# Kernel tuning notes

Hardware: AMD Instinct MI355X
Metric: run time of the kernel (lower is better)

The kernel has to match this reference:

```python
import jax, jax.numpy as jnp
import numpy as np

N_NODES = 50000
N_EDGES = 800000
BATCH = 4
D = 64


def setup_inputs() -> dict:
    key = jax.random.key(0)
    ks = jax.random.split(key, 8)
    state = jax.random.normal(ks[0], (BATCH, N_NODES, D), dtype=jnp.float32)
    edge_row = jax.random.randint(ks[1], (N_EDGES,), 0, N_NODES, dtype=jnp.int32)
    edge_col = jax.random.randint(ks[2], (N_EDGES,), 0, N_NODES, dtype=jnp.int32)
    edge_weight = jax.random.uniform(ks[3], (N_EDGES,), dtype=jnp.float32)
    stdv = 1.0 / np.sqrt(D)
    W1 = jax.random.uniform(ks[4], (D, D), minval=-stdv, maxval=stdv, dtype=jnp.float32)
    b1 = jnp.zeros((D,), dtype=jnp.float32)
    W2 = jax.random.uniform(ks[5], (D, D), minval=-stdv, maxval=stdv, dtype=jnp.float32)
    b2 = jnp.zeros((D,), dtype=jnp.float32)
    w_out = jax.random.normal(ks[6], (D,), dtype=jnp.float32) * stdv
    return {"state": state, "edge_row": edge_row, "edge_col": edge_col,
            "edge_weight": edge_weight, "W1": W1, "b1": b1, "W2": W2,
            "b2": b2, "w_out": w_out}


def _gcn_layer(x, W, bias, edge_row, edge_col, edge_weight, n, b):
    # x: [n, b, d_in] -> support [n, b, d_out]
    support = jnp.einsum('nbk,kp->nbp', x, W) + bias
    flat = support.reshape(n, -1)  # [n, b*d_out]
    # sparse spmm: out[i] = sum_{e: row_e=i} w_e * flat[col_e]
    msgs = edge_weight[:, None] * flat[edge_col]  # [E, b*d_out]
    out = jax.ops.segment_sum(msgs, edge_row, num_segments=n)
    return jax.nn.relu(out.reshape(n, b, -1))


def reference(state, edge_row, edge_col, edge_weight, W1, b1, W2, b2, w_out):
    b, n, _ = state.shape
    x = jnp.transpose(state, (1, 0, 2))  # [n, b, d]
    for W, bias in ((W1, b1), (W2, b2)):
        x = _gcn_layer(x, W, bias, edge_row, edge_col, edge_weight, n, b)
    # actor head: Linear(d,1,bias=False), squeeze, transpose -> [b, n]
    logits = jnp.einsum('nbd,d->nb', x, w_out)
    return logits.T
```

## Files before the change

kernel.cpp:

```cpp
#include <hip/hip_runtime.h>


typedef _Float16 fp16_t;
typedef _Float16 h4 __attribute__((ext_vector_type(4)));
typedef _Float16 h8 __attribute__((ext_vector_type(8)));
typedef float    f4 __attribute__((ext_vector_type(4)));
typedef unsigned long long ull;

#define CAP   64
#define RPB   256
#define BCAP  4608
#define CHK   3200
#define LROW  264
#define S1Q   (127.f / 4.f)
#define S1D   (4.f / 127.f)

__global__ __launch_bounds__(64) void prepW_k(const float* __restrict__ W,
                                              const float* __restrict__ bias,
                                              fp16_t* __restrict__ wf,
                                              float* __restrict__ bf,
                                              int* __restrict__ gcnt, int NB) {
    int lane = threadIdx.x;
    for (int i = lane; i < NB; i += 64) gcnt[i] = 0;
    int r16 = lane & 15, half = lane >> 4;
#pragma unroll
    for (int kk = 0; kk < 2; ++kk)
#pragma unroll
        for (int j = 0; j < 4; ++j) {
            h8 v;
#pragma unroll
            for (int t = 0; t < 8; ++t)
                v[t] = (_Float16)W[(32 * kk + 8 * half + t) * 64 + 16 * j + r16];
            *(h8*)&wf[((kk * 4 + j) * 64 + lane) * 8] = v;
        }
#pragma unroll
    for (int j = 0; j < 4; ++j) bf[j * 64 + lane] = bias[16 * j + r16];
}

__global__ __launch_bounds__(256) void bg_k(const int* __restrict__ erow,
                                            const int* __restrict__ ecol,
                                            const float* __restrict__ ew,
                                            int* __restrict__ gcnt,
                                            ull* __restrict__ bed,
                                            int E, int NB, int NB1,
                                            const float* __restrict__ xf,
                                            const float* __restrict__ W,
                                            const float* __restrict__ bias,
                                            unsigned char* __restrict__ flat1,
                                            int N) {
    if ((int)blockIdx.x < NB1) {
        __shared__ int hist[256], offs[256], cur[256], gbase[256];
        __shared__ ull stage[CHK];
        __shared__ unsigned short sbkt[CHK];
        int tid = threadIdx.x;
        int e0 = blockIdx.x * CHK;
        int e1 = e0 + CHK < E ? e0 + CHK : E;

        hist[tid] = 0;
        cur[tid] = 0;
        __syncthreads();
        for (int e = e0 + tid; e < e1; e += 256)
            atomicAdd(&hist[erow[e] >> 8], 1);
        __syncthreads();
        int v = hist[tid];
        offs[tid] = v;
        __syncthreads();
        for (int off = 1; off < 256; off <<= 1) {
            int t = (tid >= off) ? offs[tid - off] : 0;
            __syncthreads();
            offs[tid] += t;
            __syncthreads();
        }
        offs[tid] -= v;
        if (tid < NB && v > 0) gbase[tid] = atomicAdd(&gcnt[tid], v);
        __syncthreads();
        for (int e = e0 + tid; e < e1; e += 256) {
            int r = erow[e];
            int bk = r >> 8;
            unsigned q = (unsigned)(ew[e] * 32767.f + 0.5f);
            ull pv = ((ull)(r & 255) << 32) | (q << 17) | (unsigned)ecol[e];
            int idx = offs[bk] + atomicAdd(&cur[bk], 1);
            stage[idx] = pv;
            sbkt[idx] = (unsigned short)bk;
        }
        __syncthreads();
        int total = e1 - e0;
        for (int i = tid; i < total; i += 256) {
            int bk = sbkt[i];
            int sl = gbase[bk] + (i - offs[bk]);
            if (sl < BCAP) bed[(size_t)bk * BCAP + sl] = stage[i];
        }
    } else {
        int wave = threadIdx.x >> 6;
        int lane = threadIdx.x & 63;
        int r16 = lane & 15, half = lane >> 4;

        h8 Bf[2][4];
#pragma unroll
        for (int kk = 0; kk < 2; ++kk)
#pragma unroll
            for (int j = 0; j < 4; ++j) {
                h8 v;
#pragma unroll
                for (int t = 0; t < 8; ++t)
                    v[t] = (_Float16)W[(32 * kk + 8 * half + t) * 64 + 16 * j + r16];
                Bf[kk][j] = v;
            }
        float bj[4];
#pragma unroll
        for (int j = 0; j < 4; ++j) bj[j] = bias[16 * j + r16];

        int ntile = N >> 4;
        int gstride = gridDim.x - NB1;
        for (int tile = blockIdx.x - NB1; tile < ntile; tile += gstride) {
            int row = tile * 16 + r16;
            const float* p = xf + ((size_t)wave * N + row) * 64 + 8 * half;
            f4 u0 = *(const f4*)p;
            f4 u1 = *(const f4*)(p + 4);
            f4 u2 = *(const f4*)(p + 32);
            f4 u3 = *(const f4*)(p + 36);
            h8 A0, A1;
#pragma unroll
            for (int t = 0; t < 4; ++t) {
                A0[t] = (_Float16)u0[t]; A0[t + 4] = (_Float16)u1[t];
                A1[t] = (_Float16)u2[t]; A1[t + 4] = (_Float16)u3[t];
            }
#pragma unroll
            for (int j = 0; j < 4; ++j) {
                f4 c = {0.f, 0.f, 0.f, 0.f};
                c = __builtin_amdgcn_mfma_f32_16x16x32_f16(A0, Bf[0][j], c, 0, 0, 0);
                c = __builtin_amdgcn_mfma_f32_16x16x32_f16(A1, Bf[1][j], c, 0, 0, 0);
#pragma unroll
                for (int r = 0; r < 4; ++r) {
                    int orow = tile * 16 + 4 * half + r;
                    float fu = fmaf(c[r] + bj[j], S1Q, 128.f);
                    fu = fminf(fmaxf(fu, 0.f), 255.f);
                    flat1[(size_t)orow * 256 + wave * 64 + 16 * j + r16] =
                        (unsigned char)(fu + 0.5f);
                }
            }
        }
    }
}

__global__ __launch_bounds__(1024) void build2_k(const ull* __restrict__ bed,
                                                 const int* __restrict__ gcnt,
                                                 unsigned* __restrict__ ed,
                                                 int* __restrict__ cnt, int N) {
    __shared__ unsigned sbuf[RPB * CAP];
    __shared__ int scnt[RPB];
    int b = blockIdx.x, tid = threadIdx.x;
    for (int i = tid; i < RPB * CAP; i += 1024) sbuf[i] = 0;
    if (tid < RPB) scnt[tid] = 0;
    __syncthreads();
    int n = gcnt[b];
    n = n < BCAP ? n : BCAP;
    const ull* p = bed + (size_t)b * BCAP;
    for (int i = tid; i < n; i += 1024) {
        ull v = p[i];
        int rl = (int)(v >> 32);
        int pos = atomicAdd(&scnt[rl], 1);
        if (pos < CAP) sbuf[(rl << 6) + pos] = (unsigned)v;
    }
    __syncthreads();
    size_t base = (size_t)b * (RPB * CAP);
    for (int i = tid; i < RPB * CAP; i += 1024)
        ed[base + i] = sbuf[i];
    int r = b * RPB + tid;
    if (tid < RPB && r < N) cnt[r] = scnt[tid] < CAP ? scnt[tid] : CAP;
}

#define EDGE4I(pk, A0, A1, A2, A3, WS)                                         \
    {                                                                          \
        unsigned _p = (pk);                                                    \
        float _w = (float)(_p >> 17) * (1.f / 32767.f);                        \
        unsigned _v = *(const unsigned*)(fb + ((size_t)(_p & 0x1FFFFu) << 8)   \
                                         + lane4);                             \
        A0 += _w * (float)(_v & 0xffu);                                        \
        A1 += _w * (float)((_v >> 8) & 0xffu);                                 \
        A2 += _w * (float)((_v >> 16) & 0xffu);                                \
        A3 += _w * (float)(_v >> 24);                                          \
        WS += _w;                                                              \
    }

__global__ __launch_bounds__(256) void spmmG_k(const unsigned char* __restrict__ flat,
                                               const int* __restrict__ cnt,
                                               const unsigned* __restrict__ ed,
                                               const fp16_t* __restrict__ wf,
                                               const float* __restrict__ bf,
                                               unsigned char* __restrict__ flat2i,
                                               float* __restrict__ s2, int N) {
    __shared__ fp16_t sagg[16 * LROW];
    __shared__ h8     swf[8 * 64];
    __shared__ float  sbf[4 * 64];
    int tid  = threadIdx.x;
    int wave = tid >> 6;
    int lane = tid & 63;
    int lane4 = lane * 4;
    int r16 = lane & 15, half = lane >> 4;

    ((f4*)swf)[tid] = ((const f4*)wf)[tid];
    ((f4*)swf)[tid + 256] = ((const f4*)wf)[tid + 256];
    sbf[tid] = bf[tid];

    int blk0 = blockIdx.x * 16;
    const char* fb = (const char*)flat;
    int r0 = blk0 + wave * 4;

    int mm0 = __builtin_amdgcn_readfirstlane(cnt[r0]);
    int mm1 = __builtin_amdgcn_readfirstlane(cnt[r0 + 1]);
    int mm2 = __builtin_amdgcn_readfirstlane(cnt[r0 + 2]);
    int mm3 = __builtin_amdgcn_readfirstlane(cnt[r0 + 3]);
#define C4(a, b) ((((a) > (b) ? (a) : (b)) + 3) & ~3)
    int cA = C4(mm0, mm1) + C4(mm2, mm3);
    int cB = C4(mm0, mm2) + C4(mm1, mm3);
    int cC = C4(mm0, mm3) + C4(mm1, mm2);
    int i1, i2, i3, mI1, mI2, mI3;
    if (cA <= cB && cA <= cC) { i1 = 1; i2 = 2; i3 = 3; mI1 = mm1; mI2 = mm2; mI3 = mm3; }
    else if (cB <= cC)        { i1 = 2; i2 = 1; i3 = 3; mI1 = mm2; mI2 = mm1; mI3 = mm3; }
    else                      { i1 = 3; i2 = 1; i3 = 2; mI1 = mm3; mI2 = mm1; mI3 = mm2; }

    int pa[2] = {0, i2}, pb[2] = {i1, i3};
    int pma[2] = {mm0, mI2}, pmb[2] = {mI1, mI3};
#pragma unroll
    for (int pr = 0; pr < 2; ++pr) {
        int la = pa[pr], lb = pb[pr];
        int mr = C4(pma[pr], pmb[pr]);
        const unsigned* e0 = ed + (size_t)(r0 + la) * CAP;
        const unsigned* e1 = ed + (size_t)(r0 + lb) * CAP;
        float a0 = 0.f, a1 = 0.f, a2 = 0.f, a3 = 0.f, wsA = 0.f;
        float c0 = 0.f, c1 = 0.f, c2 = 0.f, c3 = 0.f, wsC = 0.f;
        for (int j = 0; j < mr; j += 4) {
            uint4 pA = *(const uint4*)(e0 + j);
            uint4 pB = *(const uint4*)(e1 + j);
            EDGE4I(pA.x, a0, a1, a2, a3, wsA) EDGE4I(pB.x, c0, c1, c2, c3, wsC)
            EDGE4I(pA.y, a0, a1, a2, a3, wsA) EDGE4I(pB.y, c0, c1, c2, c3, wsC)
            EDGE4I(pA.z, a0, a1, a2, a3, wsA) EDGE4I(pB.z, c0, c1, c2, c3, wsC)
            EDGE4I(pA.w, a0, a1, a2, a3, wsA) EDGE4I(pB.w, c0, c1, c2, c3, wsC)
        }
        float bA = 128.f * wsA, bC = 128.f * wsC;
        h4 s0, s1;
        s0.x = (fp16_t)fmaxf(S1D * (a0 - bA), 0.f);
        s0.y = (fp16_t)fmaxf(S1D * (a1 - bA), 0.f);
        s0.z = (fp16_t)fmaxf(S1D * (a2 - bA), 0.f);
        s0.w = (fp16_t)fmaxf(S1D * (a3 - bA), 0.f);
        s1.x = (fp16_t)fmaxf(S1D * (c0 - bC), 0.f);
        s1.y = (fp16_t)fmaxf(S1D * (c1 - bC), 0.f);
        s1.z = (fp16_t)fmaxf(S1D * (c2 - bC), 0.f);
        s1.w = (fp16_t)fmaxf(S1D * (c3 - bC), 0.f);
        *(h4*)&sagg[(wave * 4 + la) * LROW + lane4] = s0;
        *(h4*)&sagg[(wave * 4 + lb) * LROW + lane4] = s1;
    }
#undef C4
    __syncthreads();

    h8 A0 = *(const h8*)&sagg[r16 * LROW + wave * 64 + 8 * half];
    h8 A1 = *(const h8*)&sagg[r16 * LROW + wave * 64 + 32 + 8 * half];
    f4 cc[4];
#pragma unroll
    for (int j = 0; j < 4; ++j) {
        f4 c = {0.f, 0.f, 0.f, 0.f};
        c = __builtin_amdgcn_mfma_f32_16x16x32_f16(A0, swf[j * 64 + lane], c, 0, 0, 0);
        c = __builtin_amdgcn_mfma_f32_16x16x32_f16(A1, swf[(4 + j) * 64 + lane], c, 0, 0, 0);
        float bjv = sbf[j * 64 + lane];
        c.x += bjv; c.y += bjv; c.z += bjv; c.w += bjv;
        cc[j] = c;
    }
#pragma unroll
    for (int r = 0; r < 4; ++r) {
        float m = fmaxf(fmaxf(fabsf(cc[0][r]), fabsf(cc[1][r])),
                        fmaxf(fabsf(cc[2][r]), fabsf(cc[3][r])));
        m = fmaxf(m, __shfl_xor(m, 1));
        m = fmaxf(m, __shfl_xor(m, 2));
        m = fmaxf(m, __shfl_xor(m, 4));
        m = fmaxf(m, __shfl_xor(m, 8));
        int orow = blk0 + 4 * half + r;
        float inv = (m > 0.f) ? (127.f / m) : 0.f;
        if (r16 == 0) s2[(orow << 2) | wave] = m * (1.f / 127.f);
#pragma unroll
        for (int j = 0; j < 4; ++j) {
            float q = fmaf(cc[j][r], inv, 128.f);
            flat2i[(size_t)orow * 256 + wave * 64 + 16 * j + r16] =
                (unsigned char)(q + 0.5f);
        }
    }
}

#define EDGE4Q(pk, A0, A1, A2, A3, WS)                                         \
    {                                                                          \
        unsigned _p = (pk);                                                    \
        unsigned _c = _p & 0x1FFFFu;                                           \
        float _w = (float)(_p >> 17) * (1.f / 32767.f) * s2[(_c << 2) | bsel]; \
        unsigned _v = *(const unsigned*)(fb + ((size_t)_c << 8) + lane4);      \
        A0 += _w * (float)(_v & 0xffu);                                        \
        A1 += _w * (float)((_v >> 8) & 0xffu);                                 \
        A2 += _w * (float)((_v >> 16) & 0xffu);                                \
        A3 += _w * (float)(_v >> 24);                                          \
        WS += _w;                                                              \
    }

__global__ __launch_bounds__(256) void spmm2h_k(const unsigned char* __restrict__ flat,
                                                const int* __restrict__ cnt,
                                                const unsigned* __restrict__ ed,
                                                const float* __restrict__ s2,
                                                const float* __restrict__ wout,
                                                float* __restrict__ out, int N) {
    int rowi = blockIdx.x * 4 + (int)(threadIdx.x >> 6);
    int lane = threadIdx.x & 63;
    int lane4 = lane * 4;
    int bsel = lane >> 4;
    const char* fb = (const char*)flat;
    int m = __builtin_amdgcn_readfirstlane(cnt[rowi]);
    int mr = (m + 7) & ~7;
    const unsigned* ep = ed + (size_t)rowi * CAP;
    float a0 = 0.f, a1 = 0.f, a2 = 0.f, a3 = 0.f, ws = 0.f;
    for (int j = 0; j < mr; j += 8) {
        uint4 pA = *(const uint4*)(ep + j);
        uint4 pB = *(const uint4*)(ep + j + 4);
        EDGE4Q(pA.x, a0, a1, a2, a3, ws) EDGE4Q(pA.y, a0, a1, a2, a3, ws)
        EDGE4Q(pA.z, a0, a1, a2, a3, ws) EDGE4Q(pA.w, a0, a1, a2, a3, ws)
        EDGE4Q(pB.x, a0, a1, a2, a3, ws) EDGE4Q(pB.y, a0, a1, a2, a3, ws)
        EDGE4Q(pB.z, a0, a1, a2, a3, ws) EDGE4Q(pB.w, a0, a1, a2, a3, ws)
    }
    float bs = 128.f * ws;
    int t = lane & 15;
    float4 wo = ((const float4*)wout)[t];
    float p = fmaxf(a0 - bs, 0.f) * wo.x + fmaxf(a1 - bs, 0.f) * wo.y +
              fmaxf(a2 - bs, 0.f) * wo.z + fmaxf(a3 - bs, 0.f) * wo.w;
    p += __shfl_xor(p, 1); p += __shfl_xor(p, 2);
    p += __shfl_xor(p, 4); p += __shfl_xor(p, 8);
    if (t == 0) out[(size_t)bsel * N + rowi] = p;
}

extern "C" void kernel_launch(void* const* d_in, const int* in_sizes, int n_in,
                              void* d_out, int out_size, void* d_ws, size_t ws_size,
                              hipStream_t stream) {
    const float* state = (const float*)d_in[0];
    const int*   erow  = (const int*)d_in[1];
    const int*   ecol  = (const int*)d_in[2];
    const float* ew    = (const float*)d_in[3];
    const float* W1    = (const float*)d_in[4];
    const float* b1    = (const float*)d_in[5];
    const float* W2    = (const float*)d_in[6];
    const float* b2    = (const float*)d_in[7];
    const float* wout  = (const float*)d_in[8];
    float* out = (float*)d_out;

    int N = in_sizes[0] / (4 * 64);
    int E = in_sizes[1];
    int NB = (N + RPB - 1) / RPB;

    char* ws = (char*)d_ws;
    size_t off = 0;
    auto alloc = [&](size_t bytes) -> char* {
        char* p = ws + off;
        off += (bytes + 255) & ~(size_t)255;
        return p;
    };
    unsigned char* flat1  = (unsigned char*)alloc((size_t)N * 256);
    unsigned char* flat2i = (unsigned char*)alloc((size_t)N * 256);
    float*    s2    = (float*)alloc((size_t)N * 4 * 4);
    int*      cnt   = (int*)alloc((size_t)NB * RPB * 4);
    unsigned* ed    = (unsigned*)alloc((size_t)NB * RPB * CAP * 4);
    int*      gcnt  = (int*)alloc((size_t)NB * 4);
    ull*      bed   = (ull*)alloc((size_t)NB * BCAP * 8);
    fp16_t*   wf    = (fp16_t*)alloc(8 * 64 * 8 * 2);
    float*    bfr   = (float*)alloc(4 * 64 * 4);
    if (off > ws_size) return;

    prepW_k<<<1, 64, 0, stream>>>(W2, b2, wf, bfr, gcnt, NB);
    int nblk1 = (E + CHK - 1) / CHK;
    bg_k<<<nblk1 + 1024, 256, 0, stream>>>(erow, ecol, ew, gcnt, bed, E, NB,
                                           nblk1, state, W1, b1, flat1, N);
    build2_k<<<NB, 1024, 0, stream>>>(bed, gcnt, ed, cnt, N);
    spmmG_k<<<N / 16, 256, 0, stream>>>(flat1, cnt, ed, wf, bfr, flat2i, s2, N);
    spmm2h_k<<<(N + 3) / 4, 256, 0, stream>>>(flat2i, cnt, ed, s2, wout, out, N);
}
```

Baseline: 106.2 us.

## Fold W2 prep into bg_k, precompute per-row weight sums, drop per-edge scale multiplies

The separate prepW_k launch is removed. The W2/bias fp16 repacking now runs in an extra block of bg_k, and gcnt is zeroed with hipMemsetAsync. build2_k now accumulates each row's quantized edge-weight sum into a new sumq buffer, so spmmG_k no longer keeps a per-edge weight-sum accumulator. The 1/32767 dequant factor is folded into the final scale constants and into s2, which removes a multiply per edge in both SpMM kernels. The cost is an extra LDS atomic per edge in build2_k and a memset launch in place of the kernel launch. The weight sum now also includes edges beyond CAP, which the kept edge list drops.

```diff
diff --git a/kernel.cpp b/kernel.cpp
--- a/kernel.cpp
+++ b/kernel.cpp
@@ -14,28 +14,7 @@
 #define LROW  264
 #define S1Q   (127.f / 4.f)
 #define S1D   (4.f / 127.f)
-
-__global__ __launch_bounds__(64) void prepW_k(const float* __restrict__ W,
-                                              const float* __restrict__ bias,
-                                              fp16_t* __restrict__ wf,
-                                              float* __restrict__ bf,
-                                              int* __restrict__ gcnt, int NB) {
-    int lane = threadIdx.x;
-    for (int i = lane; i < NB; i += 64) gcnt[i] = 0;
-    int r16 = lane & 15, half = lane >> 4;
-#pragma unroll
-    for (int kk = 0; kk < 2; ++kk)
-#pragma unroll
-        for (int j = 0; j < 4; ++j) {
-            h8 v;
-#pragma unroll
-            for (int t = 0; t < 8; ++t)
-                v[t] = (_Float16)W[(32 * kk + 8 * half + t) * 64 + 16 * j + r16];
-            *(h8*)&wf[((kk * 4 + j) * 64 + lane) * 8] = v;
-        }
-#pragma unroll
-    for (int j = 0; j < 4; ++j) bf[j * 64 + lane] = bias[16 * j + r16];
-}
+#define SC1   (4.f / (127.f * 32767.f))
 
 __global__ __launch_bounds__(256) void bg_k(const int* __restrict__ erow,
                                             const int* __restrict__ ecol,
@@ -44,10 +23,33 @@
                                             ull* __restrict__ bed,
                                             int E, int NB, int NB1,
                                             const float* __restrict__ xf,
-                                            const float* __restrict__ W,
-                                            const float* __restrict__ bias,
+                                            const float* __restrict__ W1,
+                                            const float* __restrict__ b1,
                                             unsigned char* __restrict__ flat1,
+                                            const float* __restrict__ W2,
+                                            const float* __restrict__ b2,
+                                            fp16_t* __restrict__ wf,
+                                            float* __restrict__ bf,
                                             int N) {
+    if ((int)blockIdx.x == NB1) {
+        int lane = threadIdx.x;
+        if (lane < 64) {
+            int r16 = lane & 15, half = lane >> 4;
+#pragma unroll
+            for (int kk = 0; kk < 2; ++kk)
+#pragma unroll
+                for (int j = 0; j < 4; ++j) {
+                    h8 v;
+#pragma unroll
+                    for (int t = 0; t < 8; ++t)
+                        v[t] = (_Float16)W2[(32 * kk + 8 * half + t) * 64 + 16 * j + r16];
+                    *(h8*)&wf[((kk * 4 + j) * 64 + lane) * 8] = v;
+                }
+#pragma unroll
+            for (int j = 0; j < 4; ++j) bf[j * 64 + lane] = b2[16 * j + r16];
+        }
+        return;
+    }
     if ((int)blockIdx.x < NB1) {
         __shared__ int hist[256], offs[256], cur[256], gbase[256];
         __shared__ ull stage[CHK];
@@ -103,16 +105,16 @@
                 h8 v;
 #pragma unroll
                 for (int t = 0; t < 8; ++t)
-                    v[t] = (_Float16)W[(32 * kk + 8 * half + t) * 64 + 16 * j + r16];
+                    v[t] = (_Float16)W1[(32 * kk + 8 * half + t) * 64 + 16 * j + r16];
                 Bf[kk][j] = v;
             }
         float bj[4];
 #pragma unroll
-        for (int j = 0; j < 4; ++j) bj[j] = bias[16 * j + r16];
+        for (int j = 0; j < 4; ++j) bj[j] = b1[16 * j + r16];
 
         int ntile = N >> 4;
-        int gstride = gridDim.x - NB1;
-        for (int tile = blockIdx.x - NB1; tile < ntile; tile += gstride) {
+        int gstride = gridDim.x - NB1 - 1;
+        for (int tile = blockIdx.x - NB1 - 1; tile < ntile; tile += gstride) {
             int row = tile * 16 + r16;
             const float* p = xf + ((size_t)wave * N + row) * 64 + 8 * half;
             f4 u0 = *(const f4*)p;
@@ -146,12 +148,14 @@
 __global__ __launch_bounds__(1024) void build2_k(const ull* __restrict__ bed,
                                                  const int* __restrict__ gcnt,
                                                  unsigned* __restrict__ ed,
-                                                 int* __restrict__ cnt, int N) {
+                                                 int* __restrict__ cnt,
+                                                 int* __restrict__ sumq, int N) {
     __shared__ unsigned sbuf[RPB * CAP];
     __shared__ int scnt[RPB];
+    __shared__ int ssum[RPB];
     int b = blockIdx.x, tid = threadIdx.x;
     for (int i = tid; i < RPB * CAP; i += 1024) sbuf[i] = 0;
-    if (tid < RPB) scnt[tid] = 0;
+    if (tid < RPB) { scnt[tid] = 0; ssum[tid] = 0; }
     __syncthreads();
     int n = gcnt[b];
     n = n < BCAP ? n : BCAP;
@@ -159,32 +163,37 @@
     for (int i = tid; i < n; i += 1024) {
         ull v = p[i];
         int rl = (int)(v >> 32);
+        unsigned pk = (unsigned)v;
         int pos = atomicAdd(&scnt[rl], 1);
-        if (pos < CAP) sbuf[(rl << 6) + pos] = (unsigned)v;
+        if (pos < CAP) sbuf[(rl << 6) + pos] = pk;
+        atomicAdd(&ssum[rl], (int)(pk >> 17));
     }
     __syncthreads();
     size_t base = (size_t)b * (RPB * CAP);
     for (int i = tid; i < RPB * CAP; i += 1024)
         ed[base + i] = sbuf[i];
     int r = b * RPB + tid;
-    if (tid < RPB && r < N) cnt[r] = scnt[tid] < CAP ? scnt[tid] : CAP;
-}
-
-#define EDGE4I(pk, A0, A1, A2, A3, WS)                                         \
+    if (tid < RPB && r < N) {
+        cnt[r] = scnt[tid] < CAP ? scnt[tid] : CAP;
+        sumq[r] = ssum[tid];
+    }
+}
+
+#define EDGE4I(pk, A0, A1, A2, A3)                                             \
     {                                                                          \
         unsigned _p = (pk);                                                    \
-        float _w = (float)(_p >> 17) * (1.f / 32767.f);                        \
+        float _w = (float)(_p >> 17);                                          \
         unsigned _v = *(const unsigned*)(fb + ((size_t)(_p & 0x1FFFFu) << 8)   \
                                          + lane4);                             \
         A0 += _w * (float)(_v & 0xffu);                                        \
         A1 += _w * (float)((_v >> 8) & 0xffu);                                 \
         A2 += _w * (float)((_v >> 16) & 0xffu);                                \
         A3 += _w * (float)(_v >> 24);                                          \
-        WS += _w;                                                              \
     }
 
 __global__ __launch_bounds__(256) void spmmG_k(const unsigned char* __restrict__ flat,
                                                const int* __restrict__ cnt,
+                                               const int* __restrict__ sumq,
                                                const unsigned* __restrict__ ed,
                                                const fp16_t* __restrict__ wf,
                                                const float* __restrict__ bf,
@@ -228,26 +237,27 @@
         int mr = C4(pma[pr], pmb[pr]);
         const unsigned* e0 = ed + (size_t)(r0 + la) * CAP;
         const unsigned* e1 = ed + (size_t)(r0 + lb) * CAP;
-        float a0 = 0.f, a1 = 0.f, a2 = 0.f, a3 = 0.f, wsA = 0.f;
-        float c0 = 0.f, c1 = 0.f, c2 = 0.f, c3 = 0.f, wsC = 0.f;
+        float a0 = 0.f, a1 = 0.f, a2 = 0.f, a3 = 0.f;
+        float c0 = 0.f, c1 = 0.f, c2 = 0.f, c3 = 0.f;
         for (int j = 0; j < mr; j += 4) {
             uint4 pA = *(const uint4*)(e0 + j);
             uint4 pB = *(const uint4*)(e1 + j);
-            EDGE4I(pA.x, a0, a1, a2, a3, wsA) EDGE4I(pB.x, c0, c1, c2, c3, wsC)
-            EDGE4I(pA.y, a0, a1, a2, a3, wsA) EDGE4I(pB.y, c0, c1, c2, c3, wsC)
-            EDGE4I(pA.z, a0, a1, a2, a3, wsA) EDGE4I(pB.z, c0, c1, c2, c3, wsC)
-            EDGE4I(pA.w, a0, a1, a2, a3, wsA) EDGE4I(pB.w, c0, c1, c2, c3, wsC)
-        }
-        float bA = 128.f * wsA, bC = 128.f * wsC;
+            EDGE4I(pA.x, a0, a1, a2, a3) EDGE4I(pB.x, c0, c1, c2, c3)
+            EDGE4I(pA.y, a0, a1, a2, a3) EDGE4I(pB.y, c0, c1, c2, c3)
+            EDGE4I(pA.z, a0, a1, a2, a3) EDGE4I(pB.z, c0, c1, c2, c3)
+            EDGE4I(pA.w, a0, a1, a2, a3) EDGE4I(pB.w, c0, c1, c2, c3)
+        }
+        float bA = 128.f * (float)__builtin_amdgcn_readfirstlane(sumq[r0 + la]);
+        float bC = 128.f * (float)__builtin_amdgcn_readfirstlane(sumq[r0 + lb]);
         h4 s0, s1;
-        s0.x = (fp16_t)fmaxf(S1D * (a0 - bA), 0.f);
-        s0.y = (fp16_t)fmaxf(S1D * (a1 - bA), 0.f);
-        s0.z = (fp16_t)fmaxf(S1D * (a2 - bA), 0.f);
-        s0.w = (fp16_t)fmaxf(S1D * (a3 - bA), 0.f);
-        s1.x = (fp16_t)fmaxf(S1D * (c0 - bC), 0.f);
-        s1.y = (fp16_t)fmaxf(S1D * (c1 - bC), 0.f);
-        s1.z = (fp16_t)fmaxf(S1D * (c2 - bC), 0.f);
-        s1.w = (fp16_t)fmaxf(S1D * (c3 - bC), 0.f);
+        s0.x = (fp16_t)fmaxf(SC1 * (a0 - bA), 0.f);
+        s0.y = (fp16_t)fmaxf(SC1 * (a1 - bA), 0.f);
+        s0.z = (fp16_t)fmaxf(SC1 * (a2 - bA), 0.f);
+        s0.w = (fp16_t)fmaxf(SC1 * (a3 - bA), 0.f);
+        s1.x = (fp16_t)fmaxf(SC1 * (c0 - bC), 0.f);
+        s1.y = (fp16_t)fmaxf(SC1 * (c1 - bC), 0.f);
+        s1.z = (fp16_t)fmaxf(SC1 * (c2 - bC), 0.f);
+        s1.w = (fp16_t)fmaxf(SC1 * (c3 - bC), 0.f);
         *(h4*)&sagg[(wave * 4 + la) * LROW + lane4] = s0;
         *(h4*)&sagg[(wave * 4 + lb) * LROW + lane4] = s1;
     }
@@ -276,7 +286,8 @@
         m = fmaxf(m, __shfl_xor(m, 8));
         int orow = blk0 + 4 * half + r;
         float inv = (m > 0.f) ? (127.f / m) : 0.f;
-        if (r16 == 0) s2[(orow << 2) | wave] = m * (1.f / 127.f);
+        if (r16 == 0)
+            s2[(orow << 2) | wave] = m * (1.f / (127.f * 32767.f));
 #pragma unroll
         for (int j = 0; j < 4; ++j) {
             float q = fmaf(cc[j][r], inv, 128.f);
@@ -290,7 +301,7 @@
     {                                                                          \
         unsigned _p = (pk);                                                    \
         unsigned _c = _p & 0x1FFFFu;                                           \
-        float _w = (float)(_p >> 17) * (1.f / 32767.f) * s2[(_c << 2) | bsel]; \
+        float _w = (float)(_p >> 17) * s2[(_c << 2) | bsel];                   \
         unsigned _v = *(const unsigned*)(fb + ((size_t)_c << 8) + lane4);      \
         A0 += _w * (float)(_v & 0xffu);                                        \
         A1 += _w * (float)((_v >> 8) & 0xffu);                                 \
@@ -361,6 +372,7 @@
     unsigned char* flat2i = (unsigned char*)alloc((size_t)N * 256);
     float*    s2    = (float*)alloc((size_t)N * 4 * 4);
     int*      cnt   = (int*)alloc((size_t)NB * RPB * 4);
+    int*      sumq  = (int*)alloc((size_t)NB * RPB * 4);
     unsigned* ed    = (unsigned*)alloc((size_t)NB * RPB * CAP * 4);
     int*      gcnt  = (int*)alloc((size_t)NB * 4);
     ull*      bed   = (ull*)alloc((size_t)NB * BCAP * 8);
@@ -368,11 +380,12 @@
     float*    bfr   = (float*)alloc(4 * 64 * 4);
     if (off > ws_size) return;
 
-    prepW_k<<<1, 64, 0, stream>>>(W2, b2, wf, bfr, gcnt, NB);
     int nblk1 = (E + CHK - 1) / CHK;
-    bg_k<<<nblk1 + 1024, 256, 0, stream>>>(erow, ecol, ew, gcnt, bed, E, NB,
-                                           nblk1, state, W1, b1, flat1, N);
-    build2_k<<<NB, 1024, 0, stream>>>(bed, gcnt, ed, cnt, N);
-    spmmG_k<<<N / 16, 256, 0, stream>>>(flat1, cnt, ed, wf, bfr, flat2i, s2, N);
+    hipMemsetAsync(gcnt, 0, (size_t)NB * 4, stream);
+    bg_k<<<nblk1 + 1 + 1024, 256, 0, stream>>>(erow, ecol, ew, gcnt, bed, E, NB,
+                                               nblk1, state, W1, b1, flat1,
+                                               W2, b2, wf, bfr, N);
+    build2_k<<<NB, 1024, 0, stream>>>(bed, gcnt, ed, cnt, sumq, N);
+    spmmG_k<<<N / 16, 256, 0, stream>>>(flat1, cnt, sumq, ed, wf, bfr, flat2i, s2, N);
     spmm2h_k<<<(N + 3) / 4, 256, 0, stream>>>(flat2i, cnt, ed, s2, wout, out, N);
 }
```

New measurement: 109.9 us. +3.5%, slower.
